# Performance work log

Measured on AMD Instinct MI355X. Metric: run time of the kernel, lower is better.

Reference implementation:

```python
import jax, jax.numpy as jnp
import numpy as np

B, S, D = 4, 4096, 1024
DK, DV = 64, 64

def setup_inputs() -> dict:
    key = jax.random.key(0)
    ks = jax.random.split(key, 4)
    scale = 1.0 / np.sqrt(D)
    x = jax.random.normal(ks[0], (B, S, D), dtype=jnp.float32)
    Wq = jax.random.normal(ks[1], (DK, D), dtype=jnp.float32) * scale
    Wk = jax.random.normal(ks[2], (DK, D), dtype=jnp.float32) * scale
    Wv = jax.random.normal(ks[3], (DV, D), dtype=jnp.float32) * scale
    bq = jnp.zeros((DK,), jnp.float32)
    bk = jnp.zeros((DK,), jnp.float32)
    bv = jnp.zeros((DV,), jnp.float32)
    return {"x": x, "Wq": Wq, "bq": bq, "Wk": Wk, "bk": bk, "Wv": Wv, "bv": bv}

def reference(x, Wq, bq, Wk, bk, Wv, bv):
    # Linear projections (torch nn.Linear: y = x @ W.T + b)
    Q = jnp.einsum('bsd,kd->bsk', x, Wq) + bq      # [B,S,DK]
    K = jnp.einsum('bsd,kd->bsk', x, Wk) + bk      # [B,S,DK]
    V = jnp.einsum('bsd,vd->bsv', x, Wv) + bv      # [B,S,DV]
    scale = 1.0 / jnp.sqrt(jnp.float32(DK))
    scores = jnp.einsum('bqk,bsk->bqs', Q, K) * scale  # [B,S,S]
    attn = jax.nn.softmax(scores, axis=-1)
    return jnp.einsum('bqs,bsv->bqv', attn, V)     # [B,S,DV]
```

## Files before the change

kernel.cpp:

```cpp
#include <hip/hip_runtime.h>

typedef unsigned int uint;
typedef unsigned short ushort;

#define SQ 4096
#define DMODEL 1024
#define DH 64
#define NQ 16384
#define QSCALE (0.125f * 1.4426950408889634f)

typedef __attribute__((ext_vector_type(4))) float f32x4;
typedef __attribute__((ext_vector_type(8))) short bf16x8;


__device__ __forceinline__ void ld_lds16(const ushort* g, ushort* l) {
    __builtin_amdgcn_global_load_lds(
        (const __attribute__((address_space(1))) void*)g,
        (__attribute__((address_space(3))) void*)l, 16, 0, 0);
}

__device__ __forceinline__ uint pack2trunc(float a, float b) {
#if __has_builtin(__builtin_amdgcn_perm)
    return __builtin_amdgcn_perm(__float_as_uint(b), __float_as_uint(a),
                                 0x07060302u);
#else
    return (__float_as_uint(a) >> 16) | (__float_as_uint(b) & 0xffff0000u);
#endif
}

__device__ __forceinline__ ushort bf16rne(float a) {
    uint ua = __float_as_uint(a);
    return (ushort)((ua + 0x7fffu + ((ua >> 16) & 1u)) >> 16);
}

__device__ __forceinline__ uint bfpack_rne(float a, float b) {
    uint ua = __float_as_uint(a);
    ua = (ua + 0x7fffu + ((ua >> 16) & 1u)) >> 16;
    uint ub = __float_as_uint(b);
    ub = (ub + 0x7fffu + ((ub >> 16) & 1u)) & 0xffff0000u;
    return ua | ub;
}

#if defined(__HIP_DEVICE_COMPILE__)
#define EXP2(x) __ocml_exp2_f32(x)
extern "C" __device__ float __ocml_exp2_f32(float);
#else
#define EXP2(x) exp2f(x)
#endif

__global__ __launch_bounds__(256) void wsplit_kernel(
    const float* __restrict__ Wq, const float* __restrict__ Wk,
    const float* __restrict__ Wv, ushort* __restrict__ Wch)
{
    int r = blockIdx.x;
    int k = threadIdx.x * 4;
    const float* src = (r < 64)  ? (Wq + r * DMODEL)
                     : (r < 128) ? (Wk + (r - 64) * DMODEL)
                     :             (Wv + (r - 128) * DMODEL);
    float4 v = *(const float4*)&src[k];
    ushort h[4] = {bf16rne(v.x), bf16rne(v.y), bf16rne(v.z), bf16rne(v.w)};
    int ch = k >> 6, kl = k & 63;
    int g = kl >> 3;
    int idx = ch * 12288 + r * 64 + ((g ^ (r & 7)) << 3) + (kl & 7);
    *(ushort4*)&Wch[idx] = make_ushort4(h[0], h[1], h[2], h[3]);
}

__global__ __launch_bounds__(256, 2) void proj_kernel(
    const float* __restrict__ x, const ushort* __restrict__ Wch,
    const float* __restrict__ bq, const float* __restrict__ bk,
    const float* __restrict__ bv,
    ushort* __restrict__ Qr, ushort* __restrict__ Kr, ushort* __restrict__ Vr)
{
    __shared__ ushort sm[32768];

    const int tid  = threadIdx.x;
    const int w    = tid >> 6;
    const int l    = tid & 63;
    const int ln   = l & 15;
    const int quad = l >> 4;
    const int r0   = blockIdx.x << 5;
    const int xr   = tid >> 3;
    const int xs   = tid & 7;
    const int xidx = xr * 64 + ((xs ^ (xr & 7)) << 3);

    f32x4 o_[2][3];
    #pragma unroll
    for (int mt = 0; mt < 2; ++mt)
        #pragma unroll
        for (int nt = 0; nt < 3; ++nt) o_[mt][nt] = (f32x4)0.f;

    float4 xa, xb;
    xa = *(const float4*)&x[(r0 + xr) * DMODEL + xs * 8];
    xb = *(const float4*)&x[(r0 + xr) * DMODEL + xs * 8 + 4];
    {
        const ushort* gh = Wch + w * 3072 + l * 8;
        ushort* dh = sm + 8192 + w * 3072;
        #pragma unroll
        for (int i = 0; i < 6; ++i) ld_lds16(gh + i * 512, dh + i * 512);
    }
    {
        float f[8] = {xa.x, xa.y, xa.z, xa.w, xb.x, xb.y, xb.z, xb.w};
        uint hh[4], ll[4];
        #pragma unroll
        for (int n = 0; n < 4; ++n) {
            float a = f[2 * n], b = f[2 * n + 1];
            float la = a - __uint_as_float(__float_as_uint(a) & 0xffff0000u);
            float lb = b - __uint_as_float(__float_as_uint(b) & 0xffff0000u);
            hh[n] = pack2trunc(a, b);
            ll[n] = pack2trunc(la, lb);
        }
        *(uint4*)&sm[xidx]        = make_uint4(hh[0], hh[1], hh[2], hh[3]);
        *(uint4*)&sm[2048 + xidx] = make_uint4(ll[0], ll[1], ll[2], ll[3]);
    }

    for (int ch = 0; ch < 16; ++ch) {
        const int cur = ch & 1, nxt = cur ^ 1;
        __syncthreads();
        if (ch + 1 < 16) {
            xa = *(const float4*)&x[(r0 + xr) * DMODEL + (ch + 1) * 64 + xs * 8];
            xb = *(const float4*)&x[(r0 + xr) * DMODEL + (ch + 1) * 64 + xs * 8 + 4];
            const ushort* gh = Wch + (ch + 1) * 12288 + w * 3072 + l * 8;
            ushort* dh = sm + 8192 + nxt * 12288 + w * 3072;
            #pragma unroll
            for (int i = 0; i < 6; ++i) ld_lds16(gh + i * 512, dh + i * 512);
        }
        const ushort* Xh = sm + cur * 4096;
        const ushort* Xl = Xh + 2048;
        const ushort* Wh = sm + 8192 + cur * 12288;
        #pragma unroll
        for (int kc = 0; kc < 2; ++kc) {
            int gsw = ((kc * 4 + quad) ^ (ln & 7)) << 3;
            bf16x8 xh[2], xl[2], wh[3];
            #pragma unroll
            for (int mt = 0; mt < 2; ++mt) {
                int off = (mt * 16 + ln) * 64 + gsw;
                xh[mt] = *(bf16x8*)&Xh[off];
                xl[mt] = *(bf16x8*)&Xl[off];
            }
            #pragma unroll
            for (int nt = 0; nt < 3; ++nt)
                wh[nt] = *(bf16x8*)&Wh[(w * 48 + nt * 16 + ln) * 64 + gsw];
            #pragma unroll
            for (int mt = 0; mt < 2; ++mt)
                #pragma unroll
                for (int nt = 0; nt < 3; ++nt) {
                    o_[mt][nt] = __builtin_amdgcn_mfma_f32_16x16x32_bf16(
                        xh[mt], wh[nt], o_[mt][nt], 0, 0, 0);
                    o_[mt][nt] = __builtin_amdgcn_mfma_f32_16x16x32_bf16(
                        xl[mt], wh[nt], o_[mt][nt], 0, 0, 0);
                }
        }
        if (ch + 1 < 16) {
            float f[8] = {xa.x, xa.y, xa.z, xa.w, xb.x, xb.y, xb.z, xb.w};
            uint hh[4], ll[4];
            #pragma unroll
            for (int n = 0; n < 4; ++n) {
                float a = f[2 * n], b = f[2 * n + 1];
                float la = a - __uint_as_float(__float_as_uint(a) & 0xffff0000u);
                float lb = b - __uint_as_float(__float_as_uint(b) & 0xffff0000u);
                hh[n] = pack2trunc(a, b);
                ll[n] = pack2trunc(la, lb);
            }
            *(uint4*)&sm[nxt * 4096 + xidx] =
                make_uint4(hh[0], hh[1], hh[2], hh[3]);
            *(uint4*)&sm[nxt * 4096 + 2048 + xidx] =
                make_uint4(ll[0], ll[1], ll[2], ll[3]);
        }
    }

    __syncthreads();
    uint* Oqk = (uint*)sm;
    uint* Ov  = (uint*)sm + 4096;
    #pragma unroll
    for (int nt = 0; nt < 3; ++nt) {
        int col = 16 * (3 * w + nt) + ln;
        float bias, scl;
        if (col < 64)       { bias = bq[col];       scl = QSCALE; }
        else if (col < 128) { bias = bk[col - 64];  scl = 1.f; }
        else                { bias = bv[col - 128]; scl = 1.f; }
        #pragma unroll
        for (int mt = 0; mt < 2; ++mt)
            #pragma unroll
            for (int j = 0; j < 4; ++j) {
                int m = mt * 16 + quad * 4 + j;
                float val = (o_[mt][nt][j] + bias) * scl;
                if (col < 128) Oqk[m * 128 + col] = (uint)bf16rne(val);
                else {
                    int v = col - 128;
                    Ov[v * 32 + (m ^ ((v & 7) << 2))] = (uint)bf16rne(val);
                }
            }
    }
    __syncthreads();
    const int tile_qk = r0 >> 6;
    const int half    = r0 & 32;
    #pragma unroll
    for (int i = 0; i < 4; ++i) {
        int id = i * 256 + tid;
        int m = id >> 5, g = id & 31;
        uint4 e = *(uint4*)&Oqk[m * 128 + g * 4];
        uint2 hh;
        hh.x = e.x | (e.y << 16);
        hh.y = e.z | (e.w << 16);
        int gg = g & 15;
        int row = half + m;
        int idx = tile_qk * 4096 + row * 64 +
                  (((gg >> 1) ^ (m & 7)) << 3) + (gg & 1) * 4;
        if (g < 16) *(uint2*)&Qr[idx] = hh;
        else        *(uint2*)&Kr[idx] = hh;
    }
    const int vt = (r0 >> 12) * 64 + ((r0 & (SQ - 1)) >> 6);
    #pragma unroll
    for (int i = 0; i < 2; ++i) {
        int id = i * 256 + tid;
        int v = id >> 3, gm = id & 7;
        uint4 e = *(uint4*)&Ov[v * 32 + ((gm ^ (v & 7)) << 2)];
        uint2 hh;
        hh.x = e.x | (e.y << 16);
        hh.y = e.z | (e.w << 16);
        int tg = (half >> 3) + (gm >> 1);
        int idx = vt * 4096 + v * 64 + ((tg ^ (v & 7)) << 3) + (gm & 1) * 4;
        *(uint2*)&Vr[idx] = hh;
    }
}

__global__ __launch_bounds__(256, 2) void attn_kernel(
    const ushort* __restrict__ Qr, const ushort* __restrict__ Kr,
    const ushort* __restrict__ Vr,
    ushort* __restrict__ opart, float* __restrict__ lpart,
    float* __restrict__ out, int ks)
{
    __shared__ ushort As[32768];

    const int tid  = threadIdx.x;
    const int w    = tid >> 6;
    const int l    = tid & 63;
    const int ln   = l & 15;
    const int quad = l >> 4;

    const int bid   = blockIdx.x;
    const int qb    = bid / ks;
    const int c     = bid - qb * ks;
    const int q0    = qb << 8;
    const int b     = q0 >> 12;
    const int chunk = SQ / ks;
    const int tile0 = (b * SQ + c * chunk) >> 6;
    const int vt0   = b * 64 + ((c * chunk) >> 6);
    const int nIter = chunk >> 6;

    {
        int kt = tile0 * 4096 + w * 1024 + l * 8;
        int vt = vt0 * 4096 + w * 1024 + l * 8;
        ld_lds16(Kr + kt,       As + w * 1024);
        ld_lds16(Kr + kt + 512, As + w * 1024 + 512);
        ld_lds16(Vr + vt,       As + 4096 + w * 1024);
        ld_lds16(Vr + vt + 512, As + 4096 + w * 1024 + 512);
    }

    bf16x8 qf[4][2];
    {
        const ushort* Qbase = Qr + (q0 >> 6) * 4096;
        #pragma unroll
        for (int nt = 0; nt < 4; ++nt)
            #pragma unroll
            for (int kc = 0; kc < 2; ++kc) {
                int row = w * 64 + nt * 16 + ln;
                int off = (row >> 6) * 4096 + (row & 63) * 64 +
                          (((kc * 4 + quad) ^ (ln & 7)) << 3);
                qf[nt][kc] = *(const bf16x8*)&Qbase[off];
            }
    }

    float l_[4] = {0.f, 0.f, 0.f, 0.f};
    f32x4 o_[4][4];
    #pragma unroll
    for (int mt = 0; mt < 4; ++mt)
        #pragma unroll
        for (int nt = 0; nt < 4; ++nt) o_[mt][nt] = (f32x4)0.f;

    for (int it = 0; it < nIter; ++it) {
        const int cur = it & 1, nxt = cur ^ 1;
        __syncthreads();
        if (it + 1 < nIter) {
            int kt = (tile0 + it + 1) * 4096 + w * 1024 + l * 8;
            int vt = (vt0 + it + 1) * 4096 + w * 1024 + l * 8;
            ushort* bb = As + nxt * 8192;
            ld_lds16(Kr + kt,       bb + w * 1024);
            ld_lds16(Kr + kt + 512, bb + w * 1024 + 512);
            ld_lds16(Vr + vt,       bb + 4096 + w * 1024);
            ld_lds16(Vr + vt + 512, bb + 4096 + w * 1024 + 512);
        }
        const ushort* Ks = As + cur * 8192;
        const ushort* Vs = Ks + 4096;
        ushort* Pw = As + 16384 + w * 4096;

        f32x4 s_[4][4];
        #pragma unroll
        for (int mt = 0; mt < 4; ++mt)
            #pragma unroll
            for (int nt = 0; nt < 4; ++nt) s_[mt][nt] = (f32x4)0.f;
        #pragma unroll
        for (int kc = 0; kc < 2; ++kc) {
            int gsw = ((kc * 4 + quad) ^ (ln & 7)) << 3;
            bf16x8 kah[4];
            #pragma unroll
            for (int mt = 0; mt < 4; ++mt)
                kah[mt] = *(bf16x8*)&Ks[(mt * 16 + ln) * 64 + gsw];
            #pragma unroll
            for (int mt = 0; mt < 4; ++mt)
                #pragma unroll
                for (int nt = 0; nt < 4; ++nt)
                    s_[mt][nt] = __builtin_amdgcn_mfma_f32_16x16x32_bf16(
                        kah[mt], qf[nt][kc], s_[mt][nt], 0, 0, 0);
        }

        #pragma unroll
        for (int nt = 0; nt < 4; ++nt) {
            #pragma unroll
            for (int mt = 0; mt < 4; ++mt)
                #pragma unroll
                for (int j = 0; j < 4; ++j) {
                    float p = EXP2(s_[mt][nt][j]);
                    s_[mt][nt][j] = p;
                    l_[nt] += p;
                }
            int q = ln + 16 * nt;
            int sw = ln & 7;
            #pragma unroll
            for (int mt = 0; mt < 4; ++mt) {
                uint2 e;
                e.x = pack2trunc(s_[mt][nt][0], s_[mt][nt][1]);
                e.y = pack2trunc(s_[mt][nt][2], s_[mt][nt][3]);
                int g = 2 * mt + (quad >> 1);
                *(uint2*)&Pw[q * 64 + ((g ^ sw) << 3) + (quad & 1) * 4] = e;
            }
        }

        #pragma unroll
        for (int kc = 0; kc < 2; ++kc) {
            int gsw = ((kc * 4 + quad) ^ (ln & 7)) << 3;
            bf16x8 vah[4], pb[4];
            #pragma unroll
            for (int mt = 0; mt < 4; ++mt)
                vah[mt] = *(bf16x8*)&Vs[(mt * 16 + ln) * 64 + gsw];
            #pragma unroll
            for (int nt = 0; nt < 4; ++nt)
                pb[nt] = *(bf16x8*)&Pw[(ln + 16 * nt) * 64 + gsw];
            #pragma unroll
            for (int mt = 0; mt < 4; ++mt)
                #pragma unroll
                for (int nt = 0; nt < 4; ++nt)
                    o_[mt][nt] = __builtin_amdgcn_mfma_f32_16x16x32_bf16(
                        vah[mt], pb[nt], o_[mt][nt], 0, 0, 0);
        }
    }

    #pragma unroll
    for (int nt = 0; nt < 4; ++nt) {
        l_[nt] += __shfl_xor(l_[nt], 16);
        l_[nt] += __shfl_xor(l_[nt], 32);
    }
    float* tr = (float*)(As + 16384 + w * 4096);
    if (ks == 1) {
        #pragma unroll
        for (int nt = 0; nt < 4; ++nt) {
            float inv = 1.f / l_[nt];
            #pragma unroll
            for (int mt = 0; mt < 4; ++mt) o_[mt][nt] *= inv;
        }
    }
    if (ks > 1 && quad == 0) {
        #pragma unroll
        for (int nt = 0; nt < 4; ++nt) {
            int qg = q0 + w * 64 + 16 * nt + ln;
            lpart[c * NQ + qg] = l_[nt];
        }
    }
    #pragma unroll
    for (int p = 0; p < 4; ++p) {
        #pragma unroll
        for (int mt = 0; mt < 4; ++mt)
            #pragma unroll
            for (int j = 0; j < 4; ++j)
                tr[(ln * 16 + ((mt * 4 + quad) ^ ln)) * 4 + j] = o_[mt][p][j];
        #pragma unroll
        for (int i2 = 0; i2 < 4; ++i2) {
            int qt = i2 * 4 + quad;
            f32x4 vv = *(f32x4*)&tr[(qt * 16 + (ln ^ qt)) * 4];
            int qg = q0 + w * 64 + p * 16 + qt;
            if (ks == 1) {
                *(f32x4*)&out[qg * DH + ln * 4] = vv;
            } else {
                uint2 e;
                e.x = bfpack_rne(vv[0], vv[1]);
                e.y = bfpack_rne(vv[2], vv[3]);
                *(uint2*)&opart[((size_t)c * NQ + qg) * DH + ln * 4] = e;
            }
        }
    }
}

__global__ __launch_bounds__(256) void attn_combine(
    const ushort* __restrict__ opart, const float* __restrict__ lpart,
    float* __restrict__ out, int ks)
{
    int id = blockIdx.x * 256 + threadIdx.x;
    int q = id >> 4, c4 = id & 15;
    float den = 0.f;
    f32x4 num = (f32x4)0.f;
    for (int c = 0; c < ks; ++c) {
        den += lpart[c * NQ + q];
        ushort4 u = *(const ushort4*)&opart[((size_t)c * NQ + q) * DH + c4 * 4];
        num[0] += __uint_as_float((uint)u.x << 16);
        num[1] += __uint_as_float((uint)u.y << 16);
        num[2] += __uint_as_float((uint)u.z << 16);
        num[3] += __uint_as_float((uint)u.w << 16);
    }
    float inv = 1.f / den;
    *(f32x4*)&out[q * DH + c4 * 4] = num * inv;
}

extern "C" void kernel_launch(void* const* d_in, const int* in_sizes, int n_in,
                              void* d_out, int out_size, void* d_ws, size_t ws_size,
                              hipStream_t stream) {
    const float* x  = (const float*)d_in[0];
    const float* Wq = (const float*)d_in[1];
    const float* bq = (const float*)d_in[2];
    const float* Wk = (const float*)d_in[3];
    const float* bk = (const float*)d_in[4];
    const float* Wv = (const float*)d_in[5];
    const float* bv = (const float*)d_in[6];
    float* out = (float*)d_out;

    const size_t n16 = (size_t)NQ * DH;
    char* p = (char*)d_ws;
    ushort* Qr = (ushort*)p;           p += n16 * 2;
    ushort* Kr = (ushort*)p;           p += n16 * 2;
    ushort* Vr = (ushort*)p;           p += n16 * 2;
    ushort* Wch = (ushort*)p;          p += 192 * 1024 * 2;

    size_t base = (size_t)(p - (char*)d_ws);
    int ks = 8;
    while (ks > 1 &&
           base + (size_t)ks * n16 * 2 + (size_t)ks * NQ * 4 > ws_size)
        ks >>= 1;

    ushort* opart = (ushort*)p;        p += (size_t)ks * n16 * 2;
    float* lpart = (float*)p;

    wsplit_kernel<<<192, 256, 0, stream>>>(Wq, Wk, Wv, Wch);
    proj_kernel<<<NQ / 32, 256, 0, stream>>>(x, Wch, bq, bk, bv, Qr, Kr, Vr);
    attn_kernel<<<(NQ / 256) * ks, 256, 0, stream>>>(
        Qr, Kr, Vr, opart, lpart, out, ks);
    if (ks > 1)
        attn_combine<<<(NQ * 16) / 256, 256, 0, stream>>>(opart, lpart, out, ks);
}
```

Measured before the change: 159.6 us.

## Fuse all four kernels into one persistent kernel with grid barriers

Merges the weight conversion, QKV projection, split-K attention and combine stages into a single 512-block kernel separated by atomic-counter grid barriers, with the split count fixed at 8. This removes three kernel launch gaps and the tail drain between stages. In exchange it depends on all 512 blocks being co-resident (two per CU at 256 threads), drops the workspace-size fallback for smaller split counts, and adds spin-wait barrier latency plus a memset launch.

```diff
diff --git a/kernel.cpp b/kernel.cpp
--- a/kernel.cpp
+++ b/kernel.cpp
@@ -7,6 +7,8 @@
 #define DMODEL 1024
 #define DH 64
 #define NQ 16384
+#define KS 8
+#define NB 512
 #define QSCALE (0.125f * 1.4426950408889634f)
 
 typedef __attribute__((ext_vector_type(4))) float f32x4;
@@ -48,109 +50,86 @@
 #define EXP2(x) exp2f(x)
 #endif
 
-__global__ __launch_bounds__(256) void wsplit_kernel(
-    const float* __restrict__ Wq, const float* __restrict__ Wk,
-    const float* __restrict__ Wv, ushort* __restrict__ Wch)
-{
-    int r = blockIdx.x;
-    int k = threadIdx.x * 4;
-    const float* src = (r < 64)  ? (Wq + r * DMODEL)
-                     : (r < 128) ? (Wk + (r - 64) * DMODEL)
-                     :             (Wv + (r - 128) * DMODEL);
-    float4 v = *(const float4*)&src[k];
-    ushort h[4] = {bf16rne(v.x), bf16rne(v.y), bf16rne(v.z), bf16rne(v.w)};
-    int ch = k >> 6, kl = k & 63;
-    int g = kl >> 3;
-    int idx = ch * 12288 + r * 64 + ((g ^ (r & 7)) << 3) + (kl & 7);
-    *(ushort4*)&Wch[idx] = make_ushort4(h[0], h[1], h[2], h[3]);
-}
-
-__global__ __launch_bounds__(256, 2) void proj_kernel(
-    const float* __restrict__ x, const ushort* __restrict__ Wch,
-    const float* __restrict__ bq, const float* __restrict__ bk,
-    const float* __restrict__ bv,
-    ushort* __restrict__ Qr, ushort* __restrict__ Kr, ushort* __restrict__ Vr)
+__device__ __forceinline__ void grid_barrier(uint* cnt, uint* flag) {
+    __syncthreads();
+    if (threadIdx.x == 0) {
+        uint old = __hip_atomic_fetch_add(cnt, 1u, __ATOMIC_ACQ_REL,
+                                          __HIP_MEMORY_SCOPE_AGENT);
+        if (old == NB - 1) {
+            __hip_atomic_store(flag, 1u, __ATOMIC_RELEASE,
+                               __HIP_MEMORY_SCOPE_AGENT);
+        } else {
+            uint f;
+            do {
+                __builtin_amdgcn_s_sleep(8);
+                f = __hip_atomic_load(flag, __ATOMIC_ACQUIRE,
+                                      __HIP_MEMORY_SCOPE_AGENT);
+            } while (f == 0u);
+        }
+    }
+    __syncthreads();
+}
+
+__global__ __launch_bounds__(256, 2) void fused_kernel(
+    const float* __restrict__ x,
+    const float* __restrict__ Wq, const float* __restrict__ bq,
+    const float* __restrict__ Wk, const float* __restrict__ bk,
+    const float* __restrict__ Wv, const float* __restrict__ bv,
+    ushort* __restrict__ Wch,
+    ushort* __restrict__ Qr, ushort* __restrict__ Kr, ushort* __restrict__ Vr,
+    ushort* __restrict__ opart, float* __restrict__ lpart,
+    float* __restrict__ out, uint* __restrict__ bar)
 {
     __shared__ ushort sm[32768];
 
     const int tid  = threadIdx.x;
+    const int bid  = blockIdx.x;
     const int w    = tid >> 6;
     const int l    = tid & 63;
     const int ln   = l & 15;
     const int quad = l >> 4;
-    const int r0   = blockIdx.x << 5;
-    const int xr   = tid >> 3;
-    const int xs   = tid & 7;
-    const int xidx = xr * 64 + ((xs ^ (xr & 7)) << 3);
-
-    f32x4 o_[2][3];
-    #pragma unroll
-    for (int mt = 0; mt < 2; ++mt)
-        #pragma unroll
-        for (int nt = 0; nt < 3; ++nt) o_[mt][nt] = (f32x4)0.f;
-
-    float4 xa, xb;
-    xa = *(const float4*)&x[(r0 + xr) * DMODEL + xs * 8];
-    xb = *(const float4*)&x[(r0 + xr) * DMODEL + xs * 8 + 4];
+
     {
-        const ushort* gh = Wch + w * 3072 + l * 8;
-        ushort* dh = sm + 8192 + w * 3072;
-        #pragma unroll
-        for (int i = 0; i < 6; ++i) ld_lds16(gh + i * 512, dh + i * 512);
+        int id = bid * 256 + tid;
+        if (id < 49152) {
+            int r = id >> 8;
+            int k = (id & 255) * 4;
+            const float* src = (r < 64)  ? (Wq + r * DMODEL)
+                             : (r < 128) ? (Wk + (r - 64) * DMODEL)
+                             :             (Wv + (r - 128) * DMODEL);
+            float4 v = *(const float4*)&src[k];
+            ushort h0 = bf16rne(v.x), h1 = bf16rne(v.y);
+            ushort h2 = bf16rne(v.z), h3 = bf16rne(v.w);
+            int ch = k >> 6, kl = k & 63;
+            int g = kl >> 3;
+            int idx = ch * 12288 + r * 64 + ((g ^ (r & 7)) << 3) + (kl & 7);
+            *(ushort4*)&Wch[idx] = make_ushort4(h0, h1, h2, h3);
+        }
     }
+    grid_barrier(bar + 0, bar + 1);
+
     {
-        float f[8] = {xa.x, xa.y, xa.z, xa.w, xb.x, xb.y, xb.z, xb.w};
-        uint hh[4], ll[4];
-        #pragma unroll
-        for (int n = 0; n < 4; ++n) {
-            float a = f[2 * n], b = f[2 * n + 1];
-            float la = a - __uint_as_float(__float_as_uint(a) & 0xffff0000u);
-            float lb = b - __uint_as_float(__float_as_uint(b) & 0xffff0000u);
-            hh[n] = pack2trunc(a, b);
-            ll[n] = pack2trunc(la, lb);
-        }
-        *(uint4*)&sm[xidx]        = make_uint4(hh[0], hh[1], hh[2], hh[3]);
-        *(uint4*)&sm[2048 + xidx] = make_uint4(ll[0], ll[1], ll[2], ll[3]);
-    }
-
-    for (int ch = 0; ch < 16; ++ch) {
-        const int cur = ch & 1, nxt = cur ^ 1;
-        __syncthreads();
-        if (ch + 1 < 16) {
-            xa = *(const float4*)&x[(r0 + xr) * DMODEL + (ch + 1) * 64 + xs * 8];
-            xb = *(const float4*)&x[(r0 + xr) * DMODEL + (ch + 1) * 64 + xs * 8 + 4];
-            const ushort* gh = Wch + (ch + 1) * 12288 + w * 3072 + l * 8;
-            ushort* dh = sm + 8192 + nxt * 12288 + w * 3072;
+        const int r0   = bid << 5;
+        const int xr   = tid >> 3;
+        const int xs   = tid & 7;
+        const int xidx = xr * 64 + ((xs ^ (xr & 7)) << 3);
+
+        f32x4 o_[2][3];
+        #pragma unroll
+        for (int mt = 0; mt < 2; ++mt)
+            #pragma unroll
+            for (int nt = 0; nt < 3; ++nt) o_[mt][nt] = (f32x4)0.f;
+
+        float4 xa, xb;
+        xa = *(const float4*)&x[(r0 + xr) * DMODEL + xs * 8];
+        xb = *(const float4*)&x[(r0 + xr) * DMODEL + xs * 8 + 4];
+        {
+            const ushort* gh = Wch + w * 3072 + l * 8;
+            ushort* dh = sm + 8192 + w * 3072;
             #pragma unroll
             for (int i = 0; i < 6; ++i) ld_lds16(gh + i * 512, dh + i * 512);
         }
-        const ushort* Xh = sm + cur * 4096;
-        const ushort* Xl = Xh + 2048;
-        const ushort* Wh = sm + 8192 + cur * 12288;
-        #pragma unroll
-        for (int kc = 0; kc < 2; ++kc) {
-            int gsw = ((kc * 4 + quad) ^ (ln & 7)) << 3;
-            bf16x8 xh[2], xl[2], wh[3];
-            #pragma unroll
-            for (int mt = 0; mt < 2; ++mt) {
-                int off = (mt * 16 + ln) * 64 + gsw;
-                xh[mt] = *(bf16x8*)&Xh[off];
-                xl[mt] = *(bf16x8*)&Xl[off];
-            }
-            #pragma unroll
-            for (int nt = 0; nt < 3; ++nt)
-                wh[nt] = *(bf16x8*)&Wh[(w * 48 + nt * 16 + ln) * 64 + gsw];
-            #pragma unroll
-            for (int mt = 0; mt < 2; ++mt)
-                #pragma unroll
-                for (int nt = 0; nt < 3; ++nt) {
-                    o_[mt][nt] = __builtin_amdgcn_mfma_f32_16x16x32_bf16(
-                        xh[mt], wh[nt], o_[mt][nt], 0, 0, 0);
-                    o_[mt][nt] = __builtin_amdgcn_mfma_f32_16x16x32_bf16(
-                        xl[mt], wh[nt], o_[mt][nt], 0, 0, 0);
-                }
-        }
-        if (ch + 1 < 16) {
+        {
             float f[8] = {xa.x, xa.y, xa.z, xa.w, xb.x, xb.y, xb.z, xb.w};
             uint hh[4], ll[4];
             #pragma unroll
@@ -161,236 +140,265 @@
                 hh[n] = pack2trunc(a, b);
                 ll[n] = pack2trunc(la, lb);
             }
-            *(uint4*)&sm[nxt * 4096 + xidx] =
-                make_uint4(hh[0], hh[1], hh[2], hh[3]);
-            *(uint4*)&sm[nxt * 4096 + 2048 + xidx] =
-                make_uint4(ll[0], ll[1], ll[2], ll[3]);
+            *(uint4*)&sm[xidx]        = make_uint4(hh[0], hh[1], hh[2], hh[3]);
+            *(uint4*)&sm[2048 + xidx] = make_uint4(ll[0], ll[1], ll[2], ll[3]);
+        }
+
+        for (int ch = 0; ch < 16; ++ch) {
+            const int cur = ch & 1, nxt = cur ^ 1;
+            __syncthreads();
+            if (ch + 1 < 16) {
+                xa = *(const float4*)&x[(r0 + xr) * DMODEL + (ch + 1) * 64 + xs * 8];
+                xb = *(const float4*)&x[(r0 + xr) * DMODEL + (ch + 1) * 64 + xs * 8 + 4];
+                const ushort* gh = Wch + (ch + 1) * 12288 + w * 3072 + l * 8;
+                ushort* dh = sm + 8192 + nxt * 12288 + w * 3072;
+                #pragma unroll
+                for (int i = 0; i < 6; ++i) ld_lds16(gh + i * 512, dh + i * 512);
+            }
+            const ushort* Xh = sm + cur * 4096;
+            const ushort* Xl = Xh + 2048;
+            const ushort* Wh = sm + 8192 + cur * 12288;
+            #pragma unroll
+            for (int kc = 0; kc < 2; ++kc) {
+                int gsw = ((kc * 4 + quad) ^ (ln & 7)) << 3;
+                bf16x8 xh[2], xl[2], wh[3];
+                #pragma unroll
+                for (int mt = 0; mt < 2; ++mt) {
+                    int off = (mt * 16 + ln) * 64 + gsw;
+                    xh[mt] = *(bf16x8*)&Xh[off];
+                    xl[mt] = *(bf16x8*)&Xl[off];
+                }
+                #pragma unroll
+                for (int nt = 0; nt < 3; ++nt)
+                    wh[nt] = *(bf16x8*)&Wh[(w * 48 + nt * 16 + ln) * 64 + gsw];
+                #pragma unroll
+                for (int mt = 0; mt < 2; ++mt)
+                    #pragma unroll
+                    for (int nt = 0; nt < 3; ++nt) {
+                        o_[mt][nt] = __builtin_amdgcn_mfma_f32_16x16x32_bf16(
+                            xh[mt], wh[nt], o_[mt][nt], 0, 0, 0);
+                        o_[mt][nt] = __builtin_amdgcn_mfma_f32_16x16x32_bf16(
+                            xl[mt], wh[nt], o_[mt][nt], 0, 0, 0);
+                    }
+            }
+            if (ch + 1 < 16) {
+                float f[8] = {xa.x, xa.y, xa.z, xa.w, xb.x, xb.y, xb.z, xb.w};
+                uint hh[4], ll[4];
+                #pragma unroll
+                for (int n = 0; n < 4; ++n) {
+                    float a = f[2 * n], b = f[2 * n + 1];
+                    float la = a - __uint_as_float(__float_as_uint(a) & 0xffff0000u);
+                    float lb = b - __uint_as_float(__float_as_uint(b) & 0xffff0000u);
+                    hh[n] = pack2trunc(a, b);
+                    ll[n] = pack2trunc(la, lb);
+                }
+                *(uint4*)&sm[nxt * 4096 + xidx] =
+                    make_uint4(hh[0], hh[1], hh[2], hh[3]);
+                *(uint4*)&sm[nxt * 4096 + 2048 + xidx] =
+                    make_uint4(ll[0], ll[1], ll[2], ll[3]);
+            }
+        }
+
+        __syncthreads();
+        uint* Oqk = (uint*)sm;
+        uint* Ov  = (uint*)sm + 4096;
+        #pragma unroll
+        for (int nt = 0; nt < 3; ++nt) {
+            int col = 16 * (3 * w + nt) + ln;
+            float bias, scl;
+            if (col < 64)       { bias = bq[col];       scl = QSCALE; }
+            else if (col < 128) { bias = bk[col - 64];  scl = 1.f; }
+            else                { bias = bv[col - 128]; scl = 1.f; }
+            #pragma unroll
+            for (int mt = 0; mt < 2; ++mt)
+                #pragma unroll
+                for (int j = 0; j < 4; ++j) {
+                    int m = mt * 16 + quad * 4 + j;
+                    float val = (o_[mt][nt][j] + bias) * scl;
+                    if (col < 128) Oqk[m * 128 + col] = (uint)bf16rne(val);
+                    else {
+                        int v = col - 128;
+                        Ov[v * 32 + (m ^ ((v & 7) << 2))] = (uint)bf16rne(val);
+                    }
+                }
+        }
+        __syncthreads();
+        const int tile_qk = r0 >> 6;
+        const int half    = r0 & 32;
+        #pragma unroll
+        for (int i = 0; i < 4; ++i) {
+            int id = i * 256 + tid;
+            int m = id >> 5, g = id & 31;
+            uint4 e = *(uint4*)&Oqk[m * 128 + g * 4];
+            uint2 hh;
+            hh.x = e.x | (e.y << 16);
+            hh.y = e.z | (e.w << 16);
+            int gg = g & 15;
+            int row = half + m;
+            int idx = tile_qk * 4096 + row * 64 +
+                      (((gg >> 1) ^ (m & 7)) << 3) + (gg & 1) * 4;
+            if (g < 16) *(uint2*)&Qr[idx] = hh;
+            else        *(uint2*)&Kr[idx] = hh;
+        }
+        const int vt = (r0 >> 12) * 64 + ((r0 & (SQ - 1)) >> 6);
+        #pragma unroll
+        for (int i = 0; i < 2; ++i) {
+            int id = i * 256 + tid;
+            int v = id >> 3, gm = id & 7;
+            uint4 e = *(uint4*)&Ov[v * 32 + ((gm ^ (v & 7)) << 2)];
+            uint2 hh;
+            hh.x = e.x | (e.y << 16);
+            hh.y = e.z | (e.w << 16);
+            int tg = (half >> 3) + (gm >> 1);
+            int idx = vt * 4096 + v * 64 + ((tg ^ (v & 7)) << 3) + (gm & 1) * 4;
+            *(uint2*)&Vr[idx] = hh;
         }
     }
-
-    __syncthreads();
-    uint* Oqk = (uint*)sm;
-    uint* Ov  = (uint*)sm + 4096;
-    #pragma unroll
-    for (int nt = 0; nt < 3; ++nt) {
-        int col = 16 * (3 * w + nt) + ln;
-        float bias, scl;
-        if (col < 64)       { bias = bq[col];       scl = QSCALE; }
-        else if (col < 128) { bias = bk[col - 64];  scl = 1.f; }
-        else                { bias = bv[col - 128]; scl = 1.f; }
-        #pragma unroll
-        for (int mt = 0; mt < 2; ++mt)
-            #pragma unroll
-            for (int j = 0; j < 4; ++j) {
-                int m = mt * 16 + quad * 4 + j;
-                float val = (o_[mt][nt][j] + bias) * scl;
-                if (col < 128) Oqk[m * 128 + col] = (uint)bf16rne(val);
-                else {
-                    int v = col - 128;
-                    Ov[v * 32 + (m ^ ((v & 7) << 2))] = (uint)bf16rne(val);
+    grid_barrier(bar + 2, bar + 3);
+
+    {
+        ushort* As = sm;
+        const int qb    = bid >> 3;
+        const int c     = bid & 7;
+        const int q0    = qb << 8;
+        const int b     = q0 >> 12;
+        const int chunk = SQ / KS;
+        const int tile0 = (b * SQ + c * chunk) >> 6;
+        const int vt0   = b * 64 + ((c * chunk) >> 6);
+        const int nIter = chunk >> 6;
+
+        {
+            int kt = tile0 * 4096 + w * 1024 + l * 8;
+            int vt = vt0 * 4096 + w * 1024 + l * 8;
+            ld_lds16(Kr + kt,       As + w * 1024);
+            ld_lds16(Kr + kt + 512, As + w * 1024 + 512);
+            ld_lds16(Vr + vt,       As + 4096 + w * 1024);
+            ld_lds16(Vr + vt + 512, As + 4096 + w * 1024 + 512);
+        }
+
+        bf16x8 qf[4][2];
+        {
+            const ushort* Qbase = Qr + (q0 >> 6) * 4096;
+            #pragma unroll
+            for (int nt = 0; nt < 4; ++nt)
+                #pragma unroll
+                for (int kc = 0; kc < 2; ++kc) {
+                    int row = w * 64 + nt * 16 + ln;
+                    int off = (row >> 6) * 4096 + (row & 63) * 64 +
+                              (((kc * 4 + quad) ^ (ln & 7)) << 3);
+                    qf[nt][kc] = *(const bf16x8*)&Qbase[off];
                 }
-            }
-    }
-    __syncthreads();
-    const int tile_qk = r0 >> 6;
-    const int half    = r0 & 32;
-    #pragma unroll
-    for (int i = 0; i < 4; ++i) {
-        int id = i * 256 + tid;
-        int m = id >> 5, g = id & 31;
-        uint4 e = *(uint4*)&Oqk[m * 128 + g * 4];
-        uint2 hh;
-        hh.x = e.x | (e.y << 16);
-        hh.y = e.z | (e.w << 16);
-        int gg = g & 15;
-        int row = half + m;
-        int idx = tile_qk * 4096 + row * 64 +
-                  (((gg >> 1) ^ (m & 7)) << 3) + (gg & 1) * 4;
-        if (g < 16) *(uint2*)&Qr[idx] = hh;
-        else        *(uint2*)&Kr[idx] = hh;
-    }
-    const int vt = (r0 >> 12) * 64 + ((r0 & (SQ - 1)) >> 6);
-    #pragma unroll
-    for (int i = 0; i < 2; ++i) {
-        int id = i * 256 + tid;
-        int v = id >> 3, gm = id & 7;
-        uint4 e = *(uint4*)&Ov[v * 32 + ((gm ^ (v & 7)) << 2)];
-        uint2 hh;
-        hh.x = e.x | (e.y << 16);
-        hh.y = e.z | (e.w << 16);
-        int tg = (half >> 3) + (gm >> 1);
-        int idx = vt * 4096 + v * 64 + ((tg ^ (v & 7)) << 3) + (gm & 1) * 4;
-        *(uint2*)&Vr[idx] = hh;
-    }
-}
-
-__global__ __launch_bounds__(256, 2) void attn_kernel(
-    const ushort* __restrict__ Qr, const ushort* __restrict__ Kr,
-    const ushort* __restrict__ Vr,
-    ushort* __restrict__ opart, float* __restrict__ lpart,
-    float* __restrict__ out, int ks)
-{
-    __shared__ ushort As[32768];
-
-    const int tid  = threadIdx.x;
-    const int w    = tid >> 6;
-    const int l    = tid & 63;
-    const int ln   = l & 15;
-    const int quad = l >> 4;
-
-    const int bid   = blockIdx.x;
-    const int qb    = bid / ks;
-    const int c     = bid - qb * ks;
-    const int q0    = qb << 8;
-    const int b     = q0 >> 12;
-    const int chunk = SQ / ks;
-    const int tile0 = (b * SQ + c * chunk) >> 6;
-    const int vt0   = b * 64 + ((c * chunk) >> 6);
-    const int nIter = chunk >> 6;
-
-    {
-        int kt = tile0 * 4096 + w * 1024 + l * 8;
-        int vt = vt0 * 4096 + w * 1024 + l * 8;
-        ld_lds16(Kr + kt,       As + w * 1024);
-        ld_lds16(Kr + kt + 512, As + w * 1024 + 512);
-        ld_lds16(Vr + vt,       As + 4096 + w * 1024);
-        ld_lds16(Vr + vt + 512, As + 4096 + w * 1024 + 512);
-    }
-
-    bf16x8 qf[4][2];
-    {
-        const ushort* Qbase = Qr + (q0 >> 6) * 4096;
-        #pragma unroll
-        for (int nt = 0; nt < 4; ++nt)
+        }
+
+        float l_[4] = {0.f, 0.f, 0.f, 0.f};
+        f32x4 o_[4][4];
+        #pragma unroll
+        for (int mt = 0; mt < 4; ++mt)
+            #pragma unroll
+            for (int nt = 0; nt < 4; ++nt) o_[mt][nt] = (f32x4)0.f;
+
+        for (int it = 0; it < nIter; ++it) {
+            const int cur = it & 1, nxt = cur ^ 1;
+            __syncthreads();
+            if (it + 1 < nIter) {
+                int kt = (tile0 + it + 1) * 4096 + w * 1024 + l * 8;
+                int vt = (vt0 + it + 1) * 4096 + w * 1024 + l * 8;
+                ushort* bb = As + nxt * 8192;
+                ld_lds16(Kr + kt,       bb + w * 1024);
+                ld_lds16(Kr + kt + 512, bb + w * 1024 + 512);
+                ld_lds16(Vr + vt,       bb + 4096 + w * 1024);
+                ld_lds16(Vr + vt + 512, bb + 4096 + w * 1024 + 512);
+            }
+            const ushort* Ks = As + cur * 8192;
+            const ushort* Vs = Ks + 4096;
+            ushort* Pw = As + 16384 + w * 4096;
+
+            f32x4 s_[4][4];
+            #pragma unroll
+            for (int mt = 0; mt < 4; ++mt)
+                #pragma unroll
+                for (int nt = 0; nt < 4; ++nt) s_[mt][nt] = (f32x4)0.f;
             #pragma unroll
             for (int kc = 0; kc < 2; ++kc) {
-                int row = w * 64 + nt * 16 + ln;
-                int off = (row >> 6) * 4096 + (row & 63) * 64 +
-                          (((kc * 4 + quad) ^ (ln & 7)) << 3);
-                qf[nt][kc] = *(const bf16x8*)&Qbase[off];
-            }
-    }
-
-    float l_[4] = {0.f, 0.f, 0.f, 0.f};
-    f32x4 o_[4][4];
-    #pragma unroll
-    for (int mt = 0; mt < 4; ++mt)
-        #pragma unroll
-        for (int nt = 0; nt < 4; ++nt) o_[mt][nt] = (f32x4)0.f;
-
-    for (int it = 0; it < nIter; ++it) {
-        const int cur = it & 1, nxt = cur ^ 1;
-        __syncthreads();
-        if (it + 1 < nIter) {
-            int kt = (tile0 + it + 1) * 4096 + w * 1024 + l * 8;
-            int vt = (vt0 + it + 1) * 4096 + w * 1024 + l * 8;
-            ushort* bb = As + nxt * 8192;
-            ld_lds16(Kr + kt,       bb + w * 1024);
-            ld_lds16(Kr + kt + 512, bb + w * 1024 + 512);
-            ld_lds16(Vr + vt,       bb + 4096 + w * 1024);
-            ld_lds16(Vr + vt + 512, bb + 4096 + w * 1024 + 512);
-        }
-        const ushort* Ks = As + cur * 8192;
-        const ushort* Vs = Ks + 4096;
-        ushort* Pw = As + 16384 + w * 4096;
-
-        f32x4 s_[4][4];
-        #pragma unroll
-        for (int mt = 0; mt < 4; ++mt)
-            #pragma unroll
-            for (int nt = 0; nt < 4; ++nt) s_[mt][nt] = (f32x4)0.f;
-        #pragma unroll
-        for (int kc = 0; kc < 2; ++kc) {
-            int gsw = ((kc * 4 + quad) ^ (ln & 7)) << 3;
-            bf16x8 kah[4];
+                int gsw = ((kc * 4 + quad) ^ (ln & 7)) << 3;
+                bf16x8 kah[4];
+                #pragma unroll
+                for (int mt = 0; mt < 4; ++mt)
+                    kah[mt] = *(bf16x8*)&Ks[(mt * 16 + ln) * 64 + gsw];
+                #pragma unroll
+                for (int mt = 0; mt < 4; ++mt)
+                    #pragma unroll
+                    for (int nt = 0; nt < 4; ++nt)
+                        s_[mt][nt] = __builtin_amdgcn_mfma_f32_16x16x32_bf16(
+                            kah[mt], qf[nt][kc], s_[mt][nt], 0, 0, 0);
+            }
+
+            #pragma unroll
+            for (int nt = 0; nt < 4; ++nt) {
+                #pragma unroll
+                for (int mt = 0; mt < 4; ++mt)
+                    #pragma unroll
+                    for (int j = 0; j < 4; ++j) {
+                        float p = EXP2(s_[mt][nt][j]);
+                        s_[mt][nt][j] = p;
+                        l_[nt] += p;
+                    }
+                int q = ln + 16 * nt;
+                int sw = ln & 7;
+                #pragma unroll
+                for (int mt = 0; mt < 4; ++mt) {
+                    uint2 e;
+                    e.x = pack2trunc(s_[mt][nt][0], s_[mt][nt][1]);
+                    e.y = pack2trunc(s_[mt][nt][2], s_[mt][nt][3]);
+                    int g = 2 * mt + (quad >> 1);
+                    *(uint2*)&Pw[q * 64 + ((g ^ sw) << 3) + (quad & 1) * 4] = e;
+                }
+            }
+
+            #pragma unroll
+            for (int kc = 0; kc < 2; ++kc) {
+                int gsw = ((kc * 4 + quad) ^ (ln & 7)) << 3;
+                bf16x8 vah[4], pb[4];
+                #pragma unroll
+                for (int mt = 0; mt < 4; ++mt)
+                    vah[mt] = *(bf16x8*)&Vs[(mt * 16 + ln) * 64 + gsw];
+                #pragma unroll
+                for (int nt = 0; nt < 4; ++nt)
+                    pb[nt] = *(bf16x8*)&Pw[(ln + 16 * nt) * 64 + gsw];
+                #pragma unroll
+                for (int mt = 0; mt < 4; ++mt)
+                    #pragma unroll
+                    for (int nt = 0; nt < 4; ++nt)
+                        o_[mt][nt] = __builtin_amdgcn_mfma_f32_16x16x32_bf16(
+                            vah[mt], pb[nt], o_[mt][nt], 0, 0, 0);
+            }
+        }
+
+        #pragma unroll
+        for (int nt = 0; nt < 4; ++nt) {
+            l_[nt] += __shfl_xor(l_[nt], 16);
+            l_[nt] += __shfl_xor(l_[nt], 32);
+        }
+        if (quad == 0) {
+            #pragma unroll
+            for (int nt = 0; nt < 4; ++nt) {
+                int qg = q0 + w * 64 + 16 * nt + ln;
+                lpart[c * NQ + qg] = l_[nt];
+            }
+        }
+        float* tr = (float*)(As + 16384 + w * 4096);
+        #pragma unroll
+        for (int p = 0; p < 4; ++p) {
             #pragma unroll
             for (int mt = 0; mt < 4; ++mt)
-                kah[mt] = *(bf16x8*)&Ks[(mt * 16 + ln) * 64 + gsw];
-            #pragma unroll
-            for (int mt = 0; mt < 4; ++mt)
-                #pragma unroll
-                for (int nt = 0; nt < 4; ++nt)
-                    s_[mt][nt] = __builtin_amdgcn_mfma_f32_16x16x32_bf16(
-                        kah[mt], qf[nt][kc], s_[mt][nt], 0, 0, 0);
-        }
-
-        #pragma unroll
-        for (int nt = 0; nt < 4; ++nt) {
-            #pragma unroll
-            for (int mt = 0; mt < 4; ++mt)
-                #pragma unroll
-                for (int j = 0; j < 4; ++j) {
-                    float p = EXP2(s_[mt][nt][j]);
-                    s_[mt][nt][j] = p;
-                    l_[nt] += p;
-                }
-            int q = ln + 16 * nt;
-            int sw = ln & 7;
-            #pragma unroll
-            for (int mt = 0; mt < 4; ++mt) {
-                uint2 e;
-                e.x = pack2trunc(s_[mt][nt][0], s_[mt][nt][1]);
-                e.y = pack2trunc(s_[mt][nt][2], s_[mt][nt][3]);
-                int g = 2 * mt + (quad >> 1);
-                *(uint2*)&Pw[q * 64 + ((g ^ sw) << 3) + (quad & 1) * 4] = e;
-            }
-        }
-
-        #pragma unroll
-        for (int kc = 0; kc < 2; ++kc) {
-            int gsw = ((kc * 4 + quad) ^ (ln & 7)) << 3;
-            bf16x8 vah[4], pb[4];
-            #pragma unroll
-            for (int mt = 0; mt < 4; ++mt)
-                vah[mt] = *(bf16x8*)&Vs[(mt * 16 + ln) * 64 + gsw];
-            #pragma unroll
-            for (int nt = 0; nt < 4; ++nt)
-                pb[nt] = *(bf16x8*)&Pw[(ln + 16 * nt) * 64 + gsw];
-            #pragma unroll
-            for (int mt = 0; mt < 4; ++mt)
-                #pragma unroll
-                for (int nt = 0; nt < 4; ++nt)
-                    o_[mt][nt] = __builtin_amdgcn_mfma_f32_16x16x32_bf16(
-                        vah[mt], pb[nt], o_[mt][nt], 0, 0, 0);
-        }
-    }
-
-    #pragma unroll
-    for (int nt = 0; nt < 4; ++nt) {
-        l_[nt] += __shfl_xor(l_[nt], 16);
-        l_[nt] += __shfl_xor(l_[nt], 32);
-    }
-    float* tr = (float*)(As + 16384 + w * 4096);
-    if (ks == 1) {
-        #pragma unroll
-        for (int nt = 0; nt < 4; ++nt) {
-            float inv = 1.f / l_[nt];
-            #pragma unroll
-            for (int mt = 0; mt < 4; ++mt) o_[mt][nt] *= inv;
-        }
-    }
-    if (ks > 1 && quad == 0) {
-        #pragma unroll
-        for (int nt = 0; nt < 4; ++nt) {
-            int qg = q0 + w * 64 + 16 * nt + ln;
-            lpart[c * NQ + qg] = l_[nt];
-        }
-    }
-    #pragma unroll
-    for (int p = 0; p < 4; ++p) {
-        #pragma unroll
-        for (int mt = 0; mt < 4; ++mt)
-            #pragma unroll
-            for (int j = 0; j < 4; ++j)
-                tr[(ln * 16 + ((mt * 4 + quad) ^ ln)) * 4 + j] = o_[mt][p][j];
-        #pragma unroll
-        for (int i2 = 0; i2 < 4; ++i2) {
-            int qt = i2 * 4 + quad;
-            f32x4 vv = *(f32x4*)&tr[(qt * 16 + (ln ^ qt)) * 4];
-            int qg = q0 + w * 64 + p * 16 + qt;
-            if (ks == 1) {
-                *(f32x4*)&out[qg * DH + ln * 4] = vv;
-            } else {
+                #pragma unroll
+                for (int j = 0; j < 4; ++j)
+                    tr[(ln * 16 + ((mt * 4 + quad) ^ ln)) * 4 + j] = o_[mt][p][j];
+            #pragma unroll
+            for (int i2 = 0; i2 < 4; ++i2) {
+                int qt = i2 * 4 + quad;
+                f32x4 vv = *(f32x4*)&tr[(qt * 16 + (ln ^ qt)) * 4];
+                int qg = q0 + w * 64 + p * 16 + qt;
                 uint2 e;
                 e.x = bfpack_rne(vv[0], vv[1]);
                 e.y = bfpack_rne(vv[2], vv[3]);
@@ -398,26 +406,29 @@
             }
         }
     }
-}
-
-__global__ __launch_bounds__(256) void attn_combine(
-    const ushort* __restrict__ opart, const float* __restrict__ lpart,
-    float* __restrict__ out, int ks)
-{
-    int id = blockIdx.x * 256 + threadIdx.x;
-    int q = id >> 4, c4 = id & 15;
-    float den = 0.f;
-    f32x4 num = (f32x4)0.f;
-    for (int c = 0; c < ks; ++c) {
-        den += lpart[c * NQ + q];
-        ushort4 u = *(const ushort4*)&opart[((size_t)c * NQ + q) * DH + c4 * 4];
-        num[0] += __uint_as_float((uint)u.x << 16);
-        num[1] += __uint_as_float((uint)u.y << 16);
-        num[2] += __uint_as_float((uint)u.z << 16);
-        num[3] += __uint_as_float((uint)u.w << 16);
+    grid_barrier(bar + 4, bar + 5);
+
+    {
+        #pragma unroll
+        for (int i = 0; i < 2; ++i) {
+            int id = i * (NB * 256) + bid * 256 + tid;
+            int q = id >> 4, c4 = id & 15;
+            float den = 0.f;
+            f32x4 num = (f32x4)0.f;
+            #pragma unroll
+            for (int c = 0; c < KS; ++c) {
+                den += lpart[c * NQ + q];
+                ushort4 u = *(const ushort4*)
+                    &opart[((size_t)c * NQ + q) * DH + c4 * 4];
+                num[0] += __uint_as_float((uint)u.x << 16);
+                num[1] += __uint_as_float((uint)u.y << 16);
+                num[2] += __uint_as_float((uint)u.z << 16);
+                num[3] += __uint_as_float((uint)u.w << 16);
+            }
+            float inv = 1.f / den;
+            *(f32x4*)&out[q * DH + c4 * 4] = num * inv;
+        }
     }
-    float inv = 1.f / den;
-    *(f32x4*)&out[q * DH + c4 * 4] = num * inv;
 }
 
 extern "C" void kernel_launch(void* const* d_in, const int* in_sizes, int n_in,
@@ -438,20 +449,13 @@
     ushort* Kr = (ushort*)p;           p += n16 * 2;
     ushort* Vr = (ushort*)p;           p += n16 * 2;
     ushort* Wch = (ushort*)p;          p += 192 * 1024 * 2;
-
-    size_t base = (size_t)(p - (char*)d_ws);
-    int ks = 8;
-    while (ks > 1 &&
-           base + (size_t)ks * n16 * 2 + (size_t)ks * NQ * 4 > ws_size)
-        ks >>= 1;
-
-    ushort* opart = (ushort*)p;        p += (size_t)ks * n16 * 2;
-    float* lpart = (float*)p;
-
-    wsplit_kernel<<<192, 256, 0, stream>>>(Wq, Wk, Wv, Wch);
-    proj_kernel<<<NQ / 32, 256, 0, stream>>>(x, Wch, bq, bk, bv, Qr, Kr, Vr);
-    attn_kernel<<<(NQ / 256) * ks, 256, 0, stream>>>(
-        Qr, Kr, Vr, opart, lpart, out, ks);
-    if (ks > 1)
-        attn_combine<<<(NQ * 16) / 256, 256, 0, stream>>>(opart, lpart, out, ks);
-}
+    ushort* opart = (ushort*)p;        p += (size_t)KS * n16 * 2;
+    float* lpart = (float*)p;          p += (size_t)KS * NQ * 4;
+    uint* bar = (uint*)p;              p += 64;
+
+    hipMemsetAsync(bar, 0, 64, stream);
+
+    fused_kernel<<<NB, 256, 0, stream>>>(x, Wq, bq, Wk, bk, Wv, bv,
+                                         Wch, Qr, Kr, Vr, opart, lpart,
+                                         out, bar);
+}
```

Measured after the change: 324.3 us. 103% more time.
